# Optimization experiments

Hardware: AMD Instinct MI355X
Metric: run time of the kernel (lower is better)

## Reference

```python
import jax, jax.numpy as jnp
import numpy as np

N, E, B = 10000, 25000, 128
NF, EF, D = 32, 8, 64
STEPS = 3   # message passing steps
S2S = 3     # set2set processing steps
EPS = 1e-5

def setup_inputs() -> dict:
    key = jax.random.key(0)
    ks = jax.random.split(key, 32)
    g = lambda i, shape, scale=0.05: (jax.random.normal(ks[i], shape, dtype=jnp.float32) * scale)
    inp = {
        'x': jax.random.normal(ks[0], (N, NF), dtype=jnp.float32),
        'edge_index': jax.random.randint(ks[1], (2, E), 0, N, dtype=jnp.int32),
        'edge_attr': jax.random.normal(ks[2], (E, EF), dtype=jnp.float32),
        'batch': jnp.sort(jax.random.randint(ks[3], (N,), 0, B, dtype=jnp.int32)),
        # dense0
        'W0': g(4, (NF, D)), 'b0': jnp.zeros((D,), jnp.float32),
        # edge MLP: EF -> 2D -> D*D
        'We1': g(5, (EF, 2 * D)), 'be1': jnp.zeros((2 * D,), jnp.float32),
        'We2': g(6, (2 * D, D * D)), 'be2': jnp.zeros((D * D,), jnp.float32),
        # NNConv root weight + bias
        'root': g(7, (D, D)), 'conv_b': jnp.zeros((D,), jnp.float32),
        # GRU (input D, hidden D); gate order r, z, n (torch layout)
        'Wi': g(8, (D, 3 * D)), 'bi': jnp.zeros((3 * D,), jnp.float32),
        'Wh': g(9, (D, 3 * D)), 'bh': jnp.zeros((3 * D,), jnp.float32),
        # Set2Set LSTM (input 2D, hidden D); gate order i, f, g, o
        'Wli': g(10, (2 * D, 4 * D)), 'bli': jnp.zeros((4 * D,), jnp.float32),
        'Wlh': g(11, (D, 4 * D)), 'blh': jnp.zeros((4 * D,), jnp.float32),
        'Wr1': g(12, (2 * D, D)), 'br1': jnp.zeros((D,), jnp.float32),
        'gamma': jnp.ones((D,), jnp.float32), 'beta': jnp.zeros((D,), jnp.float32),
        'Wr2': g(13, (D, 1)), 'br2': jnp.zeros((1,), jnp.float32),
    }
    return inp

def _forward(x, edge_index, edge_attr, batch, W0, b0, We1, be1, We2, be2,
             root, conv_b, Wi, bi, Wh, bh, Wli, bli, Wlh, blh,
             Wr1, br1, gamma, beta, Wr2, br2):
    src, dst = edge_index[0], edge_index[1]
    out = jax.nn.relu(x @ W0 + b0)            # [N, D]
    h = out                                    # GRU hidden (seq_len=1)
    # edge-conditioned weights depend only on edge_attr -> compute once
    ew = (jax.nn.relu(edge_attr @ We1 + be1) @ We2 + be2).reshape(E, D, D)
    deg = jnp.maximum(jax.ops.segment_sum(jnp.ones((E,), x.dtype), dst, num_segments=N), 1.0)
    for _ in range(STEPS):
        msg = jnp.einsum('ed,edf->ef', out[src], ew)               # [E, D]
        agg = jax.ops.segment_sum(msg, dst, num_segments=N) / deg[:, None]
        m = jax.nn.relu(agg + out @ root + conv_b)                  # NNConv + relu
        # GRU cell
        gi = m @ Wi + bi
        gh = h @ Wh + bh
        ir, iz, ig = jnp.split(gi, 3, axis=-1)
        hr, hz, hg = jnp.split(gh, 3, axis=-1)
        r = jax.nn.sigmoid(ir + hr)
        z = jax.nn.sigmoid(iz + hz)
        n = jnp.tanh(ig + r * hg)
        h = (1.0 - z) * n + z * h
        out = h
    # Set2Set readout
    q_star = jnp.zeros((B, 2 * D), x.dtype)
    hl = jnp.zeros((B, D), x.dtype)
    cl = jnp.zeros((B, D), x.dtype)
    for _ in range(S2S):
        gates = q_star @ Wli + bli + hl @ Wlh + blh
        ig_, fg_, gg_, og_ = jnp.split(gates, 4, axis=-1)
        cl = jax.nn.sigmoid(fg_) * cl + jax.nn.sigmoid(ig_) * jnp.tanh(gg_)
        hl = jax.nn.sigmoid(og_) * jnp.tanh(cl)
        q = hl                                                      # [B, D]
        e = jnp.sum(out * q[batch], axis=-1)                        # [N]
        emax = jax.ops.segment_max(e, batch, num_segments=B)
        a = jnp.exp(e - emax[batch])
        a = a / jnp.maximum(jax.ops.segment_sum(a, batch, num_segments=B), 1e-12)[batch]
        r_read = jax.ops.segment_sum(a[:, None] * out, batch, num_segments=B)  # [B, D]
        q_star = jnp.concatenate([q, r_read], axis=-1)
    y = q_star @ Wr1 + br1
    mu = jnp.mean(y, axis=0)
    var = jnp.mean((y - mu) ** 2, axis=0)
    y = (y - mu) * jax.lax.rsqrt(var + EPS) * gamma + beta
    y = jax.nn.relu(y)
    y = y @ Wr2 + br2
    return y.reshape(-1)                                            # [B]

def reference(x, edge_index, edge_attr, batch, W0, b0, We1, be1, We2, be2,
              root, conv_b, Wi, bi, Wh, bh, Wli, bli, Wlh, blh,
              Wr1, br1, gamma, beta, Wr2, br2):
    return _forward(x, edge_index, edge_attr, batch, W0, b0, We1, be1, We2, be2,
                    root, conv_b, Wi, bi, Wh, bh, Wli, bli, Wlh, blh,
                    Wr1, br1, gamma, beta, Wr2, br2)
```

## Files before the change

kernel.cpp:

```cpp
#include <hip/hip_runtime.h>
#include <hip/hip_bf16.h>

constexpr int kN = 10000;
constexpr int kE = 25000;
constexpr int kB = 128;
constexpr int kNF = 32;
constexpr int kEF = 8;
constexpr int kD = 64;
constexpr int kGrp = 784;

typedef __attribute__((ext_vector_type(8))) short short8;
typedef __attribute__((ext_vector_type(4))) float floatx4;
typedef __attribute__((ext_vector_type(16))) float floatx16;

__device__ __forceinline__ unsigned short f2bf(float f) {
  unsigned u = __float_as_uint(f);
  u = (u + 0x7fffu + ((u >> 16) & 1u)) >> 16;
  return (unsigned short)u;
}
__device__ __forceinline__ float sigmf(float x) { return 1.f / (1.f + __expf(-x)); }
__device__ __forceinline__ float tanh_(float x) { return 1.f - 2.f / (__expf(2.f * x) + 1.f); }

__device__ __forceinline__ unsigned cvtpk(float lo, float hi) {
  unsigned r;
  asm("v_cvt_pk_bf16_f32 %0, %1, %2" : "=v"(r) : "v"(lo), "v"(hi));
  return r;
}

constexpr int kBlkDense = 2500;
constexpr int kBlkHid   = 12544;
constexpr int kBlkPrep  = 258;
constexpr int kBlkDeg   = 98;
constexpr int kB0H = kBlkDense;
constexpr int kB0P = kB0H + kBlkHid;
constexpr int kB0G = kB0P + kBlkPrep;
constexpr int kB0B = kB0G + kBlkDeg;
constexpr int kBlkSetup = kB0B + 1;

__global__ __launch_bounds__(256) void k_setup(
    const float* __restrict__ x, const float* __restrict__ W0, const float* __restrict__ b0,
    const float* __restrict__ ea, const float* __restrict__ We1, const float* __restrict__ be1,
    const float* __restrict__ We2, const float* __restrict__ be2,
    const int* __restrict__ ei, const int* __restrict__ batch,
    float* __restrict__ outn, unsigned short* __restrict__ hid6,
    unsigned short* __restrict__ Bc2, float* __restrict__ deg, int* __restrict__ start) {
  const int blk = blockIdx.x, t = threadIdx.x;
  if (blk < kB0H) {
    int gid = blk * 256 + t;
    int n = gid >> 6, f = gid & 63;
    float acc = b0[f];
    const float* xr = x + n * kNF;
#pragma unroll
    for (int j = 0; j < kNF; ++j) acc += xr[j] * W0[j * kD + f];
    outn[gid] = fmaxf(acc, 0.f);
  } else if (blk < kB0P) {
    int gid = (blk - kB0H) * 256 + t;
    int e_loc = gid & 31, h = (gid >> 5) & 127, grp = gid >> 12;
    int e = grp * 32 + e_loc;
    float r = 0.f;
    if (e < kE) {
      float acc = be1[h];
      const float* er = ea + e * kEF;
#pragma unroll
      for (int j = 0; j < kEF; ++j) acc += er[j] * We1[j * 128 + h];
      r = fmaxf(acc, 0.f);
    }
    hid6[gid] = f2bf(r);
  } else if (blk < kB0G) {
    int lg = (blk - kB0P) * 256 + t;
    int lane = lg & 63, slot = lg >> 6;
    int fcol, dbase;
    const float* srcmat;
    if (slot < 1024) {
      int nf_ = slot & 1, hdb = slot >> 1;
      int db = hdb & 3, h = hdb >> 2;
      fcol = nf_ * 32 + (lane & 31);
      dbase = db * 16 + (lane >> 5) * 8;
      srcmat = We2 + (size_t)h * 4096;
    } else {
      int s = slot - 1024;
      int db = s >> 1, nf_ = s & 1;
      fcol = nf_ * 32 + (lane & 31);
      dbase = db * 16 + (lane >> 5) * 8;
      srcmat = be2;
    }
    unsigned short v[8];
#pragma unroll
    for (int j = 0; j < 8; ++j) v[j] = f2bf(srcmat[(size_t)(dbase + j) * 64 + fcol]);
    *(short8*)(Bc2 + (size_t)slot * 512 + lane * 8) = *(short8*)v;
  } else if (blk < kB0B) {
    int e = (blk - kB0G) * 256 + t;
    if (e < kE) atomicAdd(&deg[ei[kE + e]], 1.f);
  } else {
    if (t > kB) return;
    int lo = 0, hi = kN;
    while (lo < hi) { int mid = (lo + hi) >> 1; if (batch[mid] < t) lo = mid + 1; else hi = mid; }
    start[t] = lo;
  }
}

__global__ __launch_bounds__(256) void k_csr(const float* __restrict__ deg,
                                             int* __restrict__ ptr) {
  __shared__ int ps[256];
  int t = threadIdx.x;
  int base = t * 40;
  int s = 0;
#pragma unroll 8
  for (int j = 0; j < 40; ++j) {
    int n = base + j;
    if (n < kN) s += (int)deg[n];
  }
  ps[t] = s;
  __syncthreads();
  for (int off = 1; off < 256; off <<= 1) {
    int v = (t >= off) ? ps[t - off] : 0;
    __syncthreads();
    ps[t] += v;
    __syncthreads();
  }
  int run = ps[t] - s;
  for (int j = 0; j < 40; ++j) {
    int n = base + j;
    if (n < kN) { ptr[n] = run; run += (int)deg[n]; }
  }
  if (t == 255) ptr[kN] = ps[255];
}

__global__ __launch_bounds__(256) void k_scatter(const int* __restrict__ ei,
    const int* __restrict__ ptr, int* __restrict__ cnt, int* __restrict__ csr) {
  int e = blockIdx.x * 256 + threadIdx.x;
  if (e < kE) {
    int d = ei[kE + e];
    int pos = atomicAdd(&cnt[d], 1);
    csr[ptr[d] + pos] = e;
  }
}

__global__ __launch_bounds__(256) void k_msg6(const int* __restrict__ ei,
    const float* __restrict__ outn, const unsigned short* __restrict__ hid6,
    const unsigned short* __restrict__ Bc2, float* __restrict__ msg) {
  __shared__ __align__(16) unsigned short hidS[128 * 32];
  __shared__ __align__(16) float res[4][32 * 64];
  const int t = threadIdx.x, lane = t & 63, wave = t >> 6;
  const int er = lane & 31, hi5 = lane >> 5;
  const int grp = blockIdx.x, e0 = grp * 32;
  {
    const char* hsrc = (const char*)(hid6 + (size_t)grp * 4096);
#pragma unroll
    for (int i = 0; i < 2; ++i) {
      int off = (wave * 2 + i) * 1024 + lane * 16;
      __builtin_amdgcn_global_load_lds(
          (const __attribute__((address_space(1))) void*)(hsrc + off),
          (__attribute__((address_space(3))) void*)((char*)hidS + off), 16, 0, 0);
    }
  }
  const int h0 = wave * 32;
  const unsigned short* bp = Bc2 + (size_t)(h0 * 8) * 512 + lane * 8;
  short8 bvr[8];
#pragma unroll
  for (int j = 0; j < 8; ++j) bvr[j] = *(const short8*)(bp + (size_t)j * 512);
  floatx4 o[4][2];
  {
    int e = e0 + er;
    int s = (e < kE) ? ei[e] : 0;
    const float* base = outn + (size_t)s * 64 + hi5 * 8;
#pragma unroll
    for (int db = 0; db < 4; ++db) {
      o[db][0] = *(const floatx4*)(base + db * 16);
      o[db][1] = *(const floatx4*)(base + db * 16 + 4);
    }
  }
  __syncthreads();

  floatx16 acc[2];
#pragma unroll
  for (int i = 0; i < 16; ++i) { acc[0][i] = 0.f; acc[1][i] = 0.f; }

  float hvc = __uint_as_float(((unsigned)hidS[h0 * 32 + er]) << 16);
  for (int hh = 0; hh < 32; ++hh) {
    unsigned short hsn = hidS[(h0 + ((hh + 1) & 31)) * 32 + er];
    const unsigned short* bpn = bp + (size_t)((hh + 1) * 8) * 512;
#pragma unroll
    for (int db = 0; db < 4; ++db) {
      short8 bv0 = bvr[db * 2], bv1 = bvr[db * 2 + 1];
      bvr[db * 2]     = *(const short8*)(bpn + (size_t)(db * 2) * 512);
      bvr[db * 2 + 1] = *(const short8*)(bpn + (size_t)(db * 2 + 1) * 512);
      floatx4 va = o[db][0] * hvc, vb = o[db][1] * hvc;
      union { uint4 u; short8 s; } U;
      U.u.x = cvtpk(va.x, va.y); U.u.y = cvtpk(va.z, va.w);
      U.u.z = cvtpk(vb.x, vb.y); U.u.w = cvtpk(vb.z, vb.w);
      acc[0] = __builtin_amdgcn_mfma_f32_32x32x16_bf16(U.s, bv0, acc[0], 0, 0, 0);
      acc[1] = __builtin_amdgcn_mfma_f32_32x32x16_bf16(U.s, bv1, acc[1], 0, 0, 0);
    }
    hvc = __uint_as_float(((unsigned)hsn) << 16);
  }
  if (wave == 3) {
#pragma unroll
    for (int db = 0; db < 4; ++db) {
      short8 bv0 = *(const short8*)(Bc2 + (size_t)(1024 + db * 2) * 512 + lane * 8);
      short8 bv1 = *(const short8*)(Bc2 + (size_t)(1024 + db * 2 + 1) * 512 + lane * 8);
      floatx4 va = o[db][0], vb = o[db][1];
      union { uint4 u; short8 s; } U;
      U.u.x = cvtpk(va.x, va.y); U.u.y = cvtpk(va.z, va.w);
      U.u.z = cvtpk(vb.x, vb.y); U.u.w = cvtpk(vb.z, vb.w);
      acc[0] = __builtin_amdgcn_mfma_f32_32x32x16_bf16(U.s, bv0, acc[0], 0, 0, 0);
      acc[1] = __builtin_amdgcn_mfma_f32_32x32x16_bf16(U.s, bv1, acc[1], 0, 0, 0);
    }
  }
#pragma unroll
  for (int nf = 0; nf < 2; ++nf)
#pragma unroll
    for (int reg = 0; reg < 16; ++reg) {
      int row = (reg & 3) + 8 * (reg >> 2) + 4 * hi5;
      res[wave][row * 64 + nf * 32 + er] = acc[nf][reg];
    }
  __syncthreads();
  int r = t >> 3, fo = (t & 7) * 8;
  float4 sA = *(const float4*)&res[0][r * 64 + fo];
  float4 sB = *(const float4*)&res[0][r * 64 + fo + 4];
#pragma unroll
  for (int w = 1; w < 4; ++w) {
    float4 aA = *(const float4*)&res[w][r * 64 + fo];
    float4 aB = *(const float4*)&res[w][r * 64 + fo + 4];
    sA.x += aA.x; sA.y += aA.y; sA.z += aA.z; sA.w += aA.w;
    sB.x += aB.x; sB.y += aB.y; sB.z += aB.z; sB.w += aB.w;
  }
  int e = e0 + r;
  if (e < kE) {
    *(float4*)(msg + (size_t)e * 64 + fo) = sA;
    *(float4*)(msg + (size_t)e * 64 + fo + 4) = sB;
  }
}

__global__ __launch_bounds__(256) void k_update(const float* __restrict__ msg,
    const int* __restrict__ ptr, const int* __restrict__ csr,
    const float* __restrict__ deg, const float* __restrict__ root,
    const float* __restrict__ convb, const float* __restrict__ Wi,
    const float* __restrict__ bi, const float* __restrict__ Wh,
    const float* __restrict__ bh, float* __restrict__ out) {
  __shared__ float sh_out[16][64];
  __shared__ float sh_m[16][64];
  int t = threadIdx.x, lane = t & 63, w = t >> 6;
  int nb = blockIdx.x * 16;
#pragma unroll
  for (int i = 0; i < 4; ++i) {
    int idx = t + i * 256;
    sh_out[idx >> 6][idx & 63] = out[(size_t)(nb + (idx >> 6)) * 64 + (idx & 63)];
  }
  __syncthreads();
  int n0 = w * 4;
  float acc[4];
#pragma unroll
  for (int i = 0; i < 4; ++i) {
    int n = nb + n0 + i;
    float dg = fmaxf(deg[n], 1.f);
    float s = 0.f;
    int p0 = ptr[n], p1 = ptr[n + 1];
    for (int k = p0; k < p1; ++k) s += msg[(size_t)csr[k] * 64 + lane];
    acc[i] = s / dg + convb[lane];
  }
  for (int d = 0; d < 64; ++d) {
    float rv = root[d * 64 + lane];
#pragma unroll
    for (int i = 0; i < 4; ++i) acc[i] += sh_out[n0 + i][d] * rv;
  }
#pragma unroll
  for (int i = 0; i < 4; ++i) sh_m[n0 + i][lane] = fmaxf(acc[i], 0.f);
  __syncthreads();
  float ir[4] = {}, iz[4] = {}, ig[4] = {}, hr[4] = {}, hz[4] = {}, hg[4] = {};
  for (int d = 0; d < 64; ++d) {
    float wi0 = Wi[d * 192 + lane], wi1 = Wi[d * 192 + 64 + lane], wi2 = Wi[d * 192 + 128 + lane];
    float wh0 = Wh[d * 192 + lane], wh1 = Wh[d * 192 + 64 + lane], wh2 = Wh[d * 192 + 128 + lane];
#pragma unroll
    for (int i = 0; i < 4; ++i) {
      float mv = sh_m[n0 + i][d], hv = sh_out[n0 + i][d];
      ir[i] += mv * wi0; iz[i] += mv * wi1; ig[i] += mv * wi2;
      hr[i] += hv * wh0; hz[i] += hv * wh1; hg[i] += hv * wh2;
    }
  }
  float bi0 = bi[lane], bi1 = bi[64 + lane], bi2 = bi[128 + lane];
  float bh0 = bh[lane], bh1 = bh[64 + lane], bh2 = bh[128 + lane];
#pragma unroll
  for (int i = 0; i < 4; ++i) {
    float r = sigmf(ir[i] + bi0 + hr[i] + bh0);
    float z = sigmf(iz[i] + bi1 + hz[i] + bh1);
    float nn = tanh_(ig[i] + bi2 + r * (hg[i] + bh2));
    float h = sh_out[n0 + i][lane];
    out[(size_t)(nb + n0 + i) * 64 + lane] = (1.f - z) * nn + z * h;
  }
}

__global__ __launch_bounds__(256) void k_s2s3(const float* __restrict__ out,
    const int* __restrict__ start, const float* __restrict__ Wli,
    const float* __restrict__ bli, const float* __restrict__ Wlh,
    const float* __restrict__ blh, const float* __restrict__ Wr1,
    const float* __restrict__ br1, float* __restrict__ y1) {
  __shared__ float qs[128], hls[64], cls[64], gates[256];
  __shared__ float ebuf[1024];
  __shared__ float part[4][64];
  __shared__ float sred[8];
  int b = blockIdx.x, t = threadIdx.x, lane = t & 63, w = t >> 6;
  if (t < 128) qs[t] = 0.f;
  if (t < 64) { hls[t] = 0.f; cls[t] = 0.f; }
  int s0 = start[b], s1 = start[b + 1];
  int cnt = s1 - s0; if (cnt > 1024) cnt = 1024;
  __syncthreads();
  for (int it = 0; it < 3; ++it) {
    float g = bli[t] + blh[t];
    for (int j = 0; j < 128; ++j) g += qs[j] * Wli[j * 256 + t];
    for (int j = 0; j < 64; ++j) g += hls[j] * Wlh[j * 256 + t];
    gates[t] = g;
    __syncthreads();
    if (t < 64) {
      float ig = sigmf(gates[t]), fg = sigmf(gates[64 + t]);
      float gg = tanh_(gates[128 + t]), og = sigmf(gates[192 + t]);
      float c = fg * cls[t] + ig * gg;
      float h = og * tanh_(c);
      cls[t] = c; hls[t] = h;
      qs[t] = h;
    }
    __syncthreads();
    for (int idx = w; idx < cnt; idx += 4) {
      int node = s0 + idx;
      float p = out[(size_t)node * 64 + lane] * hls[lane];
#pragma unroll
      for (int m = 1; m < 64; m <<= 1) p += __shfl_xor(p, m, 64);
      if (lane == 0) ebuf[idx] = p;
    }
    __syncthreads();
    float mx = -3.4e38f;
    for (int idx = t; idx < cnt; idx += 256) mx = fmaxf(mx, ebuf[idx]);
#pragma unroll
    for (int m = 1; m < 64; m <<= 1) mx = fmaxf(mx, __shfl_xor(mx, m, 64));
    if (lane == 0) sred[w] = mx;
    __syncthreads();
    mx = fmaxf(fmaxf(sred[0], sred[1]), fmaxf(sred[2], sred[3]));
    float s = 0.f;
    for (int idx = t; idx < cnt; idx += 256) {
      float a = __expf(ebuf[idx] - mx);
      ebuf[idx] = a; s += a;
    }
#pragma unroll
    for (int m = 1; m < 64; m <<= 1) s += __shfl_xor(s, m, 64);
    if (lane == 0) sred[4 + w] = s;
    __syncthreads();
    s = sred[4] + sred[5] + sred[6] + sred[7];
    float rs = 1.f / fmaxf(s, 1e-12f);
    float pr = 0.f;
    for (int idx = w; idx < cnt; idx += 4) {
      int node = s0 + idx;
      pr += ebuf[idx] * out[(size_t)node * 64 + lane];
    }
    part[w][lane] = pr;
    __syncthreads();
    if (t < 64)
      qs[64 + t] = (part[0][t] + part[1][t] + part[2][t] + part[3][t]) * rs;
    __syncthreads();
  }
  if (t < 64) {
    float acc = br1[t];
    for (int j = 0; j < 128; ++j) acc += qs[j] * Wr1[j * 64 + t];
    y1[b * 64 + t] = acc;
  }
}

__global__ __launch_bounds__(256) void k_head2(const float* __restrict__ y1,
    const float* __restrict__ gamma, const float* __restrict__ beta,
    const float* __restrict__ Wr2, const float* __restrict__ br2,
    float* __restrict__ outp) {
  __shared__ float mu[64], ri[64];
  int t = threadIdx.x;
  if (t < 64) {
    float s1 = 0.f, s2 = 0.f;
    for (int b = 0; b < kB; ++b) { float v = y1[b * 64 + t]; s1 += v; s2 += v * v; }
    float m = s1 / (float)kB;
    mu[t] = m; ri[t] = rsqrtf(s2 / (float)kB - m * m + 1e-5f);
  }
  __syncthreads();
  if (t < kB) {
    float acc = br2[0];
    for (int f = 0; f < 64; ++f) {
      float v = (y1[t * 64 + f] - mu[f]) * ri[f] * gamma[f] + beta[f];
      acc += fmaxf(v, 0.f) * Wr2[f];
    }
    outp[t] = acc;
  }
}

extern "C" void kernel_launch(void* const* d_in, const int* in_sizes, int n_in,
                              void* d_out, int out_size, void* d_ws, size_t ws_size,
                              hipStream_t stream) {
  const float* x     = (const float*)d_in[0];
  const int*   ei    = (const int*)d_in[1];
  const float* ea    = (const float*)d_in[2];
  const int*   batch = (const int*)d_in[3];
  const float* W0    = (const float*)d_in[4];
  const float* b0    = (const float*)d_in[5];
  const float* We1   = (const float*)d_in[6];
  const float* be1   = (const float*)d_in[7];
  const float* We2   = (const float*)d_in[8];
  const float* be2   = (const float*)d_in[9];
  const float* root  = (const float*)d_in[10];
  const float* convb = (const float*)d_in[11];
  const float* Wi    = (const float*)d_in[12];
  const float* bi    = (const float*)d_in[13];
  const float* Wh    = (const float*)d_in[14];
  const float* bh    = (const float*)d_in[15];
  const float* Wli   = (const float*)d_in[16];
  const float* bli   = (const float*)d_in[17];
  const float* Wlh   = (const float*)d_in[18];
  const float* blh   = (const float*)d_in[19];
  const float* Wr1   = (const float*)d_in[20];
  const float* br1   = (const float*)d_in[21];
  const float* gamma = (const float*)d_in[22];
  const float* beta  = (const float*)d_in[23];
  const float* Wr2   = (const float*)d_in[24];
  const float* br2   = (const float*)d_in[25];
  (void)in_sizes; (void)n_in; (void)out_size; (void)ws_size;

  char* ws = (char*)d_ws;
  size_t off = 0;
  auto take = [&](size_t bytes) {
    char* p = ws + off;
    off += (bytes + 255) & ~(size_t)255;
    return p;
  };
  float* deg  = (float*)take((size_t)kN * 4);
  int*   cnt  = (int*)take((size_t)kN * 4);
  size_t zeroBytes = off;
  int*   ptr   = (int*)take((size_t)(kN + 1) * 4);
  int*   csr   = (int*)take((size_t)kE * 4);
  int*   start = (int*)take(256 * 4);
  float* outn  = (float*)take((size_t)kN * kD * 4);
  float* msg   = (float*)take((size_t)kGrp * 32 * kD * 4);
  unsigned short* hid6 = (unsigned short*)take((size_t)kGrp * 4096 * 2);
  unsigned short* Bc2  = (unsigned short*)take((size_t)1032 * 512 * 2);
  float* y1    = (float*)take((size_t)kB * 64 * 4);

  hipMemsetAsync(deg, 0, zeroBytes, stream);
  k_setup<<<kBlkSetup, 256, 0, stream>>>(x, W0, b0, ea, We1, be1, We2, be2, ei, batch,
                                         outn, hid6, Bc2, deg, start);
  k_csr<<<1, 256, 0, stream>>>(deg, ptr);
  k_scatter<<<(kE + 255) / 256, 256, 0, stream>>>(ei, ptr, cnt, csr);
  for (int s = 0; s < 3; ++s) {
    k_msg6<<<kGrp, 256, 0, stream>>>(ei, outn, hid6, Bc2, msg);
    k_update<<<kN / 16, 256, 0, stream>>>(msg, ptr, csr, deg, root, convb,
                                          Wi, bi, Wh, bh, outn);
  }
  k_s2s3<<<kB, 256, 0, stream>>>(outn, start, Wli, bli, Wlh, blh, Wr1, br1, y1);
  k_head2<<<1, 256, 0, stream>>>(y1, gamma, beta, Wr2, br2, (float*)d_out);
}
```

Before: 324.4 us.

## Retile message kernel to 64 edges per block with split-K over hidden dim

After: 305.9 us. -5.7%, faster.

```diff
diff --git a/kernel.cpp b/kernel.cpp
--- a/kernel.cpp
+++ b/kernel.cpp
@@ -7,7 +7,8 @@
 constexpr int kNF = 32;
 constexpr int kEF = 8;
 constexpr int kD = 64;
-constexpr int kGrp = 784;
+constexpr int kGrp = 392;
+constexpr int kEPad = kGrp * 64;
 
 typedef __attribute__((ext_vector_type(8))) short short8;
 typedef __attribute__((ext_vector_type(4))) float floatx4;
@@ -42,7 +43,7 @@
     const float* __restrict__ ea, const float* __restrict__ We1, const float* __restrict__ be1,
     const float* __restrict__ We2, const float* __restrict__ be2,
     const int* __restrict__ ei, const int* __restrict__ batch,
-    float* __restrict__ outn, unsigned short* __restrict__ hid6,
+    float* __restrict__ outn, unsigned short* __restrict__ hid7,
     unsigned short* __restrict__ Bc2, float* __restrict__ deg, int* __restrict__ start) {
   const int blk = blockIdx.x, t = threadIdx.x;
   if (blk < kB0H) {
@@ -55,8 +56,8 @@
     outn[gid] = fmaxf(acc, 0.f);
   } else if (blk < kB0P) {
     int gid = (blk - kB0H) * 256 + t;
-    int e_loc = gid & 31, h = (gid >> 5) & 127, grp = gid >> 12;
-    int e = grp * 32 + e_loc;
+    int e_loc = gid & 63, h = (gid >> 6) & 127, grp = gid >> 13;
+    int e = grp * 64 + e_loc;
     float r = 0.f;
     if (e < kE) {
       float acc = be1[h];
@@ -65,7 +66,7 @@
       for (int j = 0; j < kEF; ++j) acc += er[j] * We1[j * 128 + h];
       r = fmaxf(acc, 0.f);
     }
-    hid6[gid] = f2bf(r);
+    hid7[gid] = f2bf(r);
   } else if (blk < kB0G) {
     int lg = (blk - kB0P) * 256 + t;
     int lane = lg & 63, slot = lg >> 6;
@@ -136,16 +137,18 @@
   }
 }
 
-__global__ __launch_bounds__(256) void k_msg6(const int* __restrict__ ei,
-    const float* __restrict__ outn, const unsigned short* __restrict__ hid6,
-    const unsigned short* __restrict__ Bc2, float* __restrict__ msg) {
-  __shared__ __align__(16) unsigned short hidS[128 * 32];
-  __shared__ __align__(16) float res[4][32 * 64];
+__global__ __launch_bounds__(256) void k_msg7(const int* __restrict__ ei,
+    const float* __restrict__ outn, const unsigned short* __restrict__ hid7,
+    const unsigned short* __restrict__ Bc2,
+    float* __restrict__ msg0, float* __restrict__ msg1) {
+  __shared__ __align__(16) unsigned short hidS[64 * 64];
+  __shared__ __align__(16) float res[4][64 * 64];
   const int t = threadIdx.x, lane = t & 63, wave = t >> 6;
   const int er = lane & 31, hi5 = lane >> 5;
-  const int grp = blockIdx.x, e0 = grp * 32;
+  const int grp = blockIdx.x, by = blockIdx.y, e0 = grp * 64;
+  float* __restrict__ msgP = by ? msg1 : msg0;
   {
-    const char* hsrc = (const char*)(hid6 + (size_t)grp * 4096);
+    const char* hsrc = (const char*)(hid7 + (size_t)grp * 8192 + by * 4096);
 #pragma unroll
     for (int i = 0; i < 2; ++i) {
       int off = (wave * 2 + i) * 1024 + lane * 16;
@@ -154,90 +157,107 @@
           (__attribute__((address_space(3))) void*)((char*)hidS + off), 16, 0, 0);
     }
   }
-  const int h0 = wave * 32;
-  const unsigned short* bp = Bc2 + (size_t)(h0 * 8) * 512 + lane * 8;
+  const int hg0 = by * 64 + wave * 16;
+  const unsigned short* bp = Bc2 + (size_t)(hg0 * 8) * 512 + lane * 8;
   short8 bvr[8];
 #pragma unroll
   for (int j = 0; j < 8; ++j) bvr[j] = *(const short8*)(bp + (size_t)j * 512);
-  floatx4 o[4][2];
-  {
-    int e = e0 + er;
+  floatx4 o[2][4][2];
+#pragma unroll
+  for (int mf = 0; mf < 2; ++mf) {
+    int e = e0 + mf * 32 + er;
     int s = (e < kE) ? ei[e] : 0;
     const float* base = outn + (size_t)s * 64 + hi5 * 8;
 #pragma unroll
     for (int db = 0; db < 4; ++db) {
-      o[db][0] = *(const floatx4*)(base + db * 16);
-      o[db][1] = *(const floatx4*)(base + db * 16 + 4);
-    }
-  }
-  __syncthreads();
-
-  floatx16 acc[2];
-#pragma unroll
-  for (int i = 0; i < 16; ++i) { acc[0][i] = 0.f; acc[1][i] = 0.f; }
-
-  float hvc = __uint_as_float(((unsigned)hidS[h0 * 32 + er]) << 16);
-  for (int hh = 0; hh < 32; ++hh) {
-    unsigned short hsn = hidS[(h0 + ((hh + 1) & 31)) * 32 + er];
+      o[mf][db][0] = *(const floatx4*)(base + db * 16);
+      o[mf][db][1] = *(const floatx4*)(base + db * 16 + 4);
+    }
+  }
+  __syncthreads();
+
+  floatx16 acc[2][2];
+#pragma unroll
+  for (int mf = 0; mf < 2; ++mf)
+#pragma unroll
+    for (int nf = 0; nf < 2; ++nf)
+#pragma unroll
+      for (int i = 0; i < 16; ++i) acc[mf][nf][i] = 0.f;
+
+  const int hl0 = wave * 16;
+#pragma unroll 2
+  for (int hh = 0; hh < 16; ++hh) {
+    int hl = hl0 + hh;
+    float hv0 = __uint_as_float(((unsigned)hidS[hl * 64 + er]) << 16);
+    float hv1 = __uint_as_float(((unsigned)hidS[hl * 64 + 32 + er]) << 16);
     const unsigned short* bpn = bp + (size_t)((hh + 1) * 8) * 512;
 #pragma unroll
     for (int db = 0; db < 4; ++db) {
       short8 bv0 = bvr[db * 2], bv1 = bvr[db * 2 + 1];
       bvr[db * 2]     = *(const short8*)(bpn + (size_t)(db * 2) * 512);
       bvr[db * 2 + 1] = *(const short8*)(bpn + (size_t)(db * 2 + 1) * 512);
-      floatx4 va = o[db][0] * hvc, vb = o[db][1] * hvc;
-      union { uint4 u; short8 s; } U;
-      U.u.x = cvtpk(va.x, va.y); U.u.y = cvtpk(va.z, va.w);
-      U.u.z = cvtpk(vb.x, vb.y); U.u.w = cvtpk(vb.z, vb.w);
-      acc[0] = __builtin_amdgcn_mfma_f32_32x32x16_bf16(U.s, bv0, acc[0], 0, 0, 0);
-      acc[1] = __builtin_amdgcn_mfma_f32_32x32x16_bf16(U.s, bv1, acc[1], 0, 0, 0);
-    }
-    hvc = __uint_as_float(((unsigned)hsn) << 16);
-  }
-  if (wave == 3) {
+      union { uint4 u; short8 s; } U0, U1;
+      floatx4 a0 = o[0][db][0] * hv0, b0 = o[0][db][1] * hv0;
+      floatx4 a1 = o[1][db][0] * hv1, b1 = o[1][db][1] * hv1;
+      U0.u.x = cvtpk(a0.x, a0.y); U0.u.y = cvtpk(a0.z, a0.w);
+      U0.u.z = cvtpk(b0.x, b0.y); U0.u.w = cvtpk(b0.z, b0.w);
+      U1.u.x = cvtpk(a1.x, a1.y); U1.u.y = cvtpk(a1.z, a1.w);
+      U1.u.z = cvtpk(b1.x, b1.y); U1.u.w = cvtpk(b1.z, b1.w);
+      acc[0][0] = __builtin_amdgcn_mfma_f32_32x32x16_bf16(U0.s, bv0, acc[0][0], 0, 0, 0);
+      acc[0][1] = __builtin_amdgcn_mfma_f32_32x32x16_bf16(U0.s, bv1, acc[0][1], 0, 0, 0);
+      acc[1][0] = __builtin_amdgcn_mfma_f32_32x32x16_bf16(U1.s, bv0, acc[1][0], 0, 0, 0);
+      acc[1][1] = __builtin_amdgcn_mfma_f32_32x32x16_bf16(U1.s, bv1, acc[1][1], 0, 0, 0);
+    }
+  }
+  if (by == 1 && wave == 3) {
 #pragma unroll
     for (int db = 0; db < 4; ++db) {
       short8 bv0 = *(const short8*)(Bc2 + (size_t)(1024 + db * 2) * 512 + lane * 8);
       short8 bv1 = *(const short8*)(Bc2 + (size_t)(1024 + db * 2 + 1) * 512 + lane * 8);
-      floatx4 va = o[db][0], vb = o[db][1];
-      union { uint4 u; short8 s; } U;
-      U.u.x = cvtpk(va.x, va.y); U.u.y = cvtpk(va.z, va.w);
-      U.u.z = cvtpk(vb.x, vb.y); U.u.w = cvtpk(vb.z, vb.w);
-      acc[0] = __builtin_amdgcn_mfma_f32_32x32x16_bf16(U.s, bv0, acc[0], 0, 0, 0);
-      acc[1] = __builtin_amdgcn_mfma_f32_32x32x16_bf16(U.s, bv1, acc[1], 0, 0, 0);
-    }
-  }
-#pragma unroll
-  for (int nf = 0; nf < 2; ++nf)
-#pragma unroll
-    for (int reg = 0; reg < 16; ++reg) {
-      int row = (reg & 3) + 8 * (reg >> 2) + 4 * hi5;
-      res[wave][row * 64 + nf * 32 + er] = acc[nf][reg];
-    }
-  __syncthreads();
-  int r = t >> 3, fo = (t & 7) * 8;
-  float4 sA = *(const float4*)&res[0][r * 64 + fo];
-  float4 sB = *(const float4*)&res[0][r * 64 + fo + 4];
-#pragma unroll
-  for (int w = 1; w < 4; ++w) {
-    float4 aA = *(const float4*)&res[w][r * 64 + fo];
-    float4 aB = *(const float4*)&res[w][r * 64 + fo + 4];
-    sA.x += aA.x; sA.y += aA.y; sA.z += aA.z; sA.w += aA.w;
-    sB.x += aB.x; sB.y += aB.y; sB.z += aB.z; sB.w += aB.w;
-  }
-  int e = e0 + r;
-  if (e < kE) {
-    *(float4*)(msg + (size_t)e * 64 + fo) = sA;
-    *(float4*)(msg + (size_t)e * 64 + fo + 4) = sB;
-  }
-}
-
-__global__ __launch_bounds__(256) void k_update(const float* __restrict__ msg,
-    const int* __restrict__ ptr, const int* __restrict__ csr,
-    const float* __restrict__ deg, const float* __restrict__ root,
-    const float* __restrict__ convb, const float* __restrict__ Wi,
-    const float* __restrict__ bi, const float* __restrict__ Wh,
-    const float* __restrict__ bh, float* __restrict__ out) {
+      union { uint4 u; short8 s; } U0, U1;
+      floatx4 a0 = o[0][db][0], b0 = o[0][db][1];
+      floatx4 a1 = o[1][db][0], b1 = o[1][db][1];
+      U0.u.x = cvtpk(a0.x, a0.y); U0.u.y = cvtpk(a0.z, a0.w);
+      U0.u.z = cvtpk(b0.x, b0.y); U0.u.w = cvtpk(b0.z, b0.w);
+      U1.u.x = cvtpk(a1.x, a1.y); U1.u.y = cvtpk(a1.z, a1.w);
+      U1.u.z = cvtpk(b1.x, b1.y); U1.u.w = cvtpk(b1.z, b1.w);
+      acc[0][0] = __builtin_amdgcn_mfma_f32_32x32x16_bf16(U0.s, bv0, acc[0][0], 0, 0, 0);
+      acc[0][1] = __builtin_amdgcn_mfma_f32_32x32x16_bf16(U0.s, bv1, acc[0][1], 0, 0, 0);
+      acc[1][0] = __builtin_amdgcn_mfma_f32_32x32x16_bf16(U1.s, bv0, acc[1][0], 0, 0, 0);
+      acc[1][1] = __builtin_amdgcn_mfma_f32_32x32x16_bf16(U1.s, bv1, acc[1][1], 0, 0, 0);
+    }
+  }
+#pragma unroll
+  for (int mf = 0; mf < 2; ++mf)
+#pragma unroll
+    for (int nf = 0; nf < 2; ++nf)
+#pragma unroll
+      for (int reg = 0; reg < 16; ++reg) {
+        int row = (reg & 3) + 8 * (reg >> 2) + 4 * hi5 + mf * 32;
+        res[wave][row * 64 + nf * 32 + er] = acc[mf][nf][reg];
+      }
+  __syncthreads();
+#pragma unroll
+  for (int q = 0; q < 4; ++q) {
+    int idx = q * 1024 + t * 4;
+    float4 s4 = *(const float4*)&res[0][idx];
+#pragma unroll
+    for (int w = 1; w < 4; ++w) {
+      float4 a4 = *(const float4*)&res[w][idx];
+      s4.x += a4.x; s4.y += a4.y; s4.z += a4.z; s4.w += a4.w;
+    }
+    int e = e0 + (idx >> 6);
+    if (e < kE) *(float4*)(msgP + (size_t)e * 64 + (idx & 63)) = s4;
+  }
+}
+
+__global__ __launch_bounds__(256) void k_update(const float* __restrict__ msg0,
+    const float* __restrict__ msg1, const int* __restrict__ ptr,
+    const int* __restrict__ csr, const float* __restrict__ deg,
+    const float* __restrict__ root, const float* __restrict__ convb,
+    const float* __restrict__ Wi, const float* __restrict__ bi,
+    const float* __restrict__ Wh, const float* __restrict__ bh,
+    float* __restrict__ out) {
   __shared__ float sh_out[16][64];
   __shared__ float sh_m[16][64];
   int t = threadIdx.x, lane = t & 63, w = t >> 6;
@@ -256,7 +276,10 @@
     float dg = fmaxf(deg[n], 1.f);
     float s = 0.f;
     int p0 = ptr[n], p1 = ptr[n + 1];
-    for (int k = p0; k < p1; ++k) s += msg[(size_t)csr[k] * 64 + lane];
+    for (int k = p0; k < p1; ++k) {
+      size_t off2 = (size_t)csr[k] * 64 + lane;
+      s += msg0[off2] + msg1[off2];
+    }
     acc[i] = s / dg + convb[lane];
   }
   for (int d = 0; d < 64; ++d) {
@@ -432,19 +455,21 @@
   int*   csr   = (int*)take((size_t)kE * 4);
   int*   start = (int*)take(256 * 4);
   float* outn  = (float*)take((size_t)kN * kD * 4);
-  float* msg   = (float*)take((size_t)kGrp * 32 * kD * 4);
-  unsigned short* hid6 = (unsigned short*)take((size_t)kGrp * 4096 * 2);
+  float* msg0  = (float*)take((size_t)kEPad * kD * 4);
+  float* msg1  = (float*)take((size_t)kEPad * kD * 4);
+  unsigned short* hid7 = (unsigned short*)take((size_t)kGrp * 8192 * 2);
   unsigned short* Bc2  = (unsigned short*)take((size_t)1032 * 512 * 2);
   float* y1    = (float*)take((size_t)kB * 64 * 4);
 
   hipMemsetAsync(deg, 0, zeroBytes, stream);
   k_setup<<<kBlkSetup, 256, 0, stream>>>(x, W0, b0, ea, We1, be1, We2, be2, ei, batch,
-                                         outn, hid6, Bc2, deg, start);
+                                         outn, hid7, Bc2, deg, start);
   k_csr<<<1, 256, 0, stream>>>(deg, ptr);
   k_scatter<<<(kE + 255) / 256, 256, 0, stream>>>(ei, ptr, cnt, csr);
+  dim3 gm(kGrp, 2);
   for (int s = 0; s < 3; ++s) {
-    k_msg6<<<kGrp, 256, 0, stream>>>(ei, outn, hid6, Bc2, msg);
-    k_update<<<kN / 16, 256, 0, stream>>>(msg, ptr, csr, deg, root, convb,
+    k_msg7<<<gm, 256, 0, stream>>>(ei, outn, hid7, Bc2, msg0, msg1);
+    k_update<<<kN / 16, 256, 0, stream>>>(msg0, msg1, ptr, csr, deg, root, convb,
                                           Wi, bi, Wh, bh, outn);
   }
   k_s2s3<<<kB, 256, 0, stream>>>(outn, start, Wli, bli, Wlh, blh, Wr1, br1, y1);
```
